# Kernel tuning notes

Measured on AMD Instinct MI355X. Metric: run time of the kernel, lower is better.

## Reference

```python
import jax, jax.numpy as jnp
import numpy as np

B, S, E, H = 2, 1024, 1024, 16
Dh = E // H


def setup_inputs() -> dict:
    key = jax.random.key(0)
    ks = jax.random.split(key, 32)
    sc = 1.0 / np.sqrt(E)  # xavier-ish scale
    inp = {}
    names_x = ["x_q_a", "x_q_b", "x_kv_a", "x_kv_b"]
    for i, n in enumerate(names_x):
        inp[n] = jax.random.normal(ks[i], (B, S, E), jnp.float32)
    # causal mask, broadcastable to (B, H, S, S); masked where == 0
    inp["mask"] = jnp.tril(jnp.ones((S, S), jnp.int32))[None, None, :, :]
    inp["layer_theta"] = jnp.float32(0.3)
    inp["thetas_head"] = 0.1 * jax.random.normal(ks[4], (H,), jnp.float32)
    i = 5
    for p in ["q", "k", "v", "o"]:
        inp[p + "_wa"] = sc * jax.random.normal(ks[i], (E, E), jnp.float32); i += 1
        inp[p + "_wb"] = sc * jax.random.normal(ks[i], (E, E), jnp.float32); i += 1
        inp[p + "_ba"] = jnp.zeros((E,), jnp.float32)
        inp[p + "_bb"] = jnp.zeros((E,), jnp.float32)
    return inp


def _qc_dense(xa, xb, wa, wb, ba, bb, j2):
    # F.linear: x @ W.T + b ; j2 is a scalar so (Wb*j2) factors out
    out_a = xa @ wa.T + ba + (xb @ wb.T) * j2
    out_b = xa @ wb.T + bb + xb @ wa.T
    return out_a, out_b


def _shape(x):
    # (B,S,E) -> (B,H,S,Dh)
    return x.reshape(B, S, H, Dh).transpose(0, 2, 1, 3)


def _unshape(x):
    return x.transpose(0, 2, 1, 3).reshape(B, S, E)


def _rope(x):
    # standard rotate-half RoPE on last dim, positions over axis -2
    inv_freq = 1.0 / (10000.0 ** (jnp.arange(0, Dh, 2, dtype=jnp.float32) / Dh))
    ang = jnp.arange(S, dtype=jnp.float32)[:, None] * inv_freq[None, :]  # (S, Dh/2)
    cos = jnp.concatenate([jnp.cos(ang), jnp.cos(ang)], axis=-1)  # (S, Dh)
    sin = jnp.concatenate([jnp.sin(ang), jnp.sin(ang)], axis=-1)
    x1, x2 = x[..., : Dh // 2], x[..., Dh // 2:]
    rot = jnp.concatenate([-x2, x1], axis=-1)
    return x * cos + rot * sin


def reference(x_q_a, x_q_b, x_kv_a, x_kv_b, mask, layer_theta, thetas_head,
              q_wa, q_wb, q_ba, q_bb, k_wa, k_wb, k_ba, k_bb,
              v_wa, v_wb, v_ba, v_bb, o_wa, o_wb, o_ba, o_bb):
    j2 = jnp.sin(2.0 * layer_theta) - 1.0
    qa, qb = _qc_dense(x_q_a, x_q_b, q_wa, q_wb, q_ba, q_bb, j2)
    ka, kb = _qc_dense(x_kv_a, x_kv_b, k_wa, k_wb, k_ba, k_bb, j2)
    va, vb = _qc_dense(x_kv_a, x_kv_b, v_wa, v_wb, v_ba, v_bb, j2)
    qa, qb = _rope(_shape(qa)), _rope(_shape(qb))
    ka, kb = _rope(_shape(ka)), _rope(_shape(kb))
    va, vb = _shape(va), _shape(vb)
    j2h = (jnp.sin(2.0 * thetas_head) - 1.0).reshape(1, H, 1, 1)
    # dual QC score matrices (B,H,S,S)
    s_a = jnp.einsum("bhqd,bhkd->bhqk", qa, ka) + jnp.einsum("bhqd,bhkd->bhqk", qb, kb) * j2h
    s_b = jnp.einsum("bhqd,bhkd->bhqk", qa, kb) + jnp.einsum("bhqd,bhkd->bhqk", qb, ka)
    mag = jnp.sqrt(s_a * s_a + s_b * s_b + 1e-8) / np.sqrt(Dh)
    mag = jnp.where(mask == 0, -1e9, mag)
    attn = jax.nn.softmax(mag, axis=-1)
    out_a = _unshape(jnp.einsum("bhqk,bhkd->bhqd", attn, va))
    out_b = _unshape(jnp.einsum("bhqk,bhkd->bhqd", attn, vb))
    return _qc_dense(out_a, out_b, o_wa, o_wb, o_ba, o_bb, j2)
```

## Files before the change

kernel.cpp:

```cpp
#include <hip/hip_runtime.h>
#include <math.h>
#include <stdint.h>

#define BATCH 2
#define SEQ   1024
#define EMB   1024
#define NH    16
#define DH    64
#define BSE   (BATCH*SEQ*EMB)
#define MROWS (BATCH*SEQ)

typedef unsigned short u16;
typedef __attribute__((ext_vector_type(8))) short short8;
typedef __attribute__((ext_vector_type(4))) float f32x4;

__device__ __forceinline__ float bf2f(u16 u) {
    return __uint_as_float(((unsigned int)u) << 16);
}
__device__ __forceinline__ u16 f2bf(float f) {
    unsigned int x = __float_as_uint(f);
    x += 0x7FFFu + ((x >> 16) & 1u);
    return (u16)(x >> 16);
}

__device__ __forceinline__ void async_copy16(const void* g, void* l) {
    __builtin_amdgcn_global_load_lds(
        (const __attribute__((address_space(1))) unsigned int*)g,
        (__attribute__((address_space(3))) unsigned int*)l,
        16, 0, 0);
}

struct PackArgs {
    const float* src[20];
    u16*         dst[20];
    int          scaled[20];
};

__global__ __launch_bounds__(256) void pack_kernel(PackArgs pa, const float* __restrict__ theta)
{
    const int e = blockIdx.y;
    const size_t i = ((size_t)blockIdx.x * 256 + threadIdx.x) * 4;
    float sc = 1.0f;
    if (pa.scaled[e]) sc = sinf(2.0f * theta[0]) - 1.0f;
    float4 v = *(const float4*)(pa.src[e] + i);
    ushort4 o;
    o.x = f2bf(v.x * sc); o.y = f2bf(v.y * sc);
    o.z = f2bf(v.z * sc); o.w = f2bf(v.w * sc);
    *(ushort4*)(pa.dst[e] + i) = o;
}

struct GemmArgs {
    const u16*   A1s[8];
    const u16*   A2s[8];
    const u16*   Blo[8];
    const u16*   Bhi[8];
    const float* bias[8];
    void*        dst[8];
    int          mode[8];
};

template<int SPLITK>
__global__ __launch_bounds__(256) void mfma_gemm(GemmArgs ga)
{
    __shared__ u16 sA[128][32];
    __shared__ u16 sB[128][32];

    const int t    = threadIdx.x;
    const int lane = t & 63;
    const int w    = t >> 6;
    const int wx   = w & 1;
    const int wy   = w >> 1;
    const int n0   = blockIdx.y * 128;
    const int m0   = blockIdx.x * 128;
    const int ko   = (SPLITK == 2) ? blockIdx.z : 0;
    const int seg  = n0 >> 10;
    const int nloc = n0 & 1023;

    const int srow = t >> 2;
    const int sb   = (t & 3) * 16;

    f32x4 acc[4][4] = {};

    const char* A1 = (const char*)ga.A1s[seg];
    const char* A2 = (const char*)ga.A2s[seg];
    const char* Bl = (const char*)ga.Blo[seg];
    const char* Bh = (const char*)ga.Bhi[seg];
    if (SPLITK == 2 && ko) { A1 = A2; Bl = Bh; }

    const int frow = lane & 15;
    const int quad = lane >> 4;

    const int NKT = (SPLITK == 2) ? 32 : 64;
    for (int kt = 0; kt < NKT; ++kt) {
        const char* As = (SPLITK == 1 && (kt & 32)) ? A2 : A1;
        const char* Bs = (SPLITK == 1 && (kt & 32)) ? Bh : Bl;
        const size_t kbyte = (size_t)(kt & 31) * 64;

        __syncthreads();
        #pragma unroll
        for (int r = 0; r < 2; ++r) {
            const int row = r*64 + srow;
            const int ldsoff = (r*64 + w*16) * 64;
            async_copy16(As + (size_t)(m0 + row)*2048 + kbyte + sb,
                         (char*)&sA[0][0] + ldsoff);
            async_copy16(Bs + (size_t)(nloc + row)*2048 + kbyte + sb,
                         (char*)&sB[0][0] + ldsoff);
        }
        __syncthreads();

        short8 af[4], bfr[4];
        #pragma unroll
        for (int i = 0; i < 4; ++i)
            af[i] = *(const short8*)&sA[wy*64 + i*16 + frow][quad*8];
        #pragma unroll
        for (int j = 0; j < 4; ++j)
            bfr[j] = *(const short8*)&sB[wx*64 + j*16 + frow][quad*8];

        #pragma unroll
        for (int i = 0; i < 4; ++i)
            #pragma unroll
            for (int j = 0; j < 4; ++j)
                acc[i][j] = __builtin_amdgcn_mfma_f32_16x16x32_bf16(
                                af[i], bfr[j], acc[i][j], 0, 0, 0);
    }

    const float* bias = ga.bias[seg];
    const int mode = ga.mode[seg];

    #pragma unroll
    for (int j = 0; j < 4; ++j) {
        const int c = nloc + wx*64 + j*16 + frow;
        const float bv = (SPLITK == 2 && ko) ? 0.0f : bias[c];
        #pragma unroll
        for (int i = 0; i < 4; ++i) {
            #pragma unroll
            for (int reg = 0; reg < 4; ++reg) {
                const int m = m0 + wy*64 + i*16 + quad*4 + reg;
                const float val = acc[i][j][reg] + bv;
                if (mode == 1) {
                    if (SPLITK == 2)
                        atomicAdd((float*)ga.dst[seg] + (size_t)m*1024 + c, val);
                    else
                        ((float*)ga.dst[seg])[(size_t)m*1024 + c] = val;
                } else if (mode == 2) {
                    ((u16*)ga.dst[seg])[((size_t)(m >> 10) << 20) + (size_t)c*1024 + (m & 1023)] = f2bf(val);
                } else {
                    ((u16*)ga.dst[seg])[(size_t)m*1024 + c] = f2bf(val);
                }
            }
        }
    }
}

__global__ __launch_bounds__(256) void rope_kernel(
    u16* qa, u16* qb, u16* ka, u16* kb)
{
    u16* p;
    switch (blockIdx.y) {
        case 0:  p = qa; break;
        case 1:  p = qb; break;
        case 2:  p = ka; break;
        default: p = kb; break;
    }
    const int i   = blockIdx.x * 256 + threadIdx.x;
    const int d   = i & 31;
    const int hh  = (i >> 5) & (NH - 1);
    const int row = i >> 9;
    const int s   = row & (SEQ - 1);
    const size_t base = (size_t)row * EMB + hh * DH;

    float x1 = bf2f(p[base + d]);
    float x2 = bf2f(p[base + d + 32]);
    const float invf_rev = expf(-(float)d * 0.28782313662425576f) * 0.15915494309189535f;
    float rev = (float)s * invf_rev;
    rev -= floorf(rev);
    const float sn = __builtin_amdgcn_sinf(rev);
    const float cs = __builtin_amdgcn_cosf(rev);
    p[base + d]      = f2bf(x1 * cs - x2 * sn);
    p[base + d + 32] = f2bf(x2 * cs + x1 * sn);
}

__global__ __launch_bounds__(256) void attn_mfma(
    const u16* __restrict__ qa, const u16* __restrict__ qb,
    const u16* __restrict__ ka, const u16* __restrict__ kb,
    const u16* __restrict__ vat, const u16* __restrict__ vbt,
    const float* __restrict__ thetas,
    u16* __restrict__ oa, u16* __restrict__ ob)
{
    __shared__ u16 sKa[64][64];
    __shared__ u16 sKb[64][64];
    __shared__ u16 sVa[64][64];
    __shared__ u16 sVb[64][64];
    __shared__ u16 sP[4][16][72];

    const int t    = threadIdx.x;
    const int lane = t & 63;
    const int w    = t >> 6;
    const int L15  = lane & 15;
    const int quad = lane >> 4;

    const int bid  = blockIdx.x;
    const int aa   = (bid >> 5) & 7;
    const int qt   = (bid >> 8) ? aa : (15 - aa);
    const int bh   = bid & 31;
    const int h    = bh & 15;
    const int b    = bh >> 4;

    const float j2h = sinf(2.0f * thetas[h]) - 1.0f;

    const int   qrow  = qt*64 + w*16 + L15;
    const size_t qbase = (size_t)(b*SEQ + qrow) * EMB + h*DH;
    short8 fqa[2], fqb[2], fjqb[2];
    fqa[0] = *(const short8*)(qa + qbase + quad*8);
    fqa[1] = *(const short8*)(qa + qbase + 32 + quad*8);
    fqb[0] = *(const short8*)(qb + qbase + quad*8);
    fqb[1] = *(const short8*)(qb + qbase + 32 + quad*8);
    #pragma unroll
    for (int s2 = 0; s2 < 2; ++s2) {
        short8 src = fqb[s2], dst;
        #pragma unroll
        for (int j = 0; j < 8; ++j)
            dst[j] = (short)f2bf(bf2f((u16)src[j]) * j2h);
        fjqb[s2] = dst;
    }

    f32x4 acc_a[4] = {};
    f32x4 acc_b[4] = {};
    float l_lane[4] = {0.f, 0.f, 0.f, 0.f};

    const int subrow = lane >> 3;
    const int g      = (lane & 7) ^ subrow;
    const int swz    = L15 & 7;

    for (int kt = 0; kt <= qt; ++kt) {
        __syncthreads();
        #pragma unroll
        for (int i = 0; i < 2; ++i) {
            const int row = w*16 + i*8 + subrow;
            const int ldsoff = (w*16 + i*8) * 128;
            const size_t ktok = (size_t)(b*SEQ + kt*64 + row);
            async_copy16((const char*)ka + ktok*2048 + h*128 + g*16,
                         (char*)&sKa[0][0] + ldsoff);
            async_copy16((const char*)kb + ktok*2048 + h*128 + g*16,
                         (char*)&sKb[0][0] + ldsoff);
            const size_t vrow = (size_t)b*1048576 + (size_t)(h*64 + row)*1024 + kt*64;
            async_copy16((const char*)vat + vrow*2 + g*16,
                         (char*)&sVa[0][0] + ldsoff);
            async_copy16((const char*)vbt + vrow*2 + g*16,
                         (char*)&sVb[0][0] + ldsoff);
        }
        __syncthreads();

        f32x4 sa[4] = {}, sb[4] = {};
        #pragma unroll
        for (int n = 0; n < 4; ++n) {
            const u16* rKa = &sKa[n*16 + L15][0];
            const u16* rKb = &sKb[n*16 + L15][0];
            short8 ka0 = *(const short8*)(rKa + (( quad      ^ swz) << 3));
            short8 ka1 = *(const short8*)(rKa + (((4 + quad) ^ swz) << 3));
            short8 kb0 = *(const short8*)(rKb + (( quad      ^ swz) << 3));
            short8 kb1 = *(const short8*)(rKb + (((4 + quad) ^ swz) << 3));
            sa[n] = __builtin_amdgcn_mfma_f32_16x16x32_bf16(fqa[0],  ka0, sa[n], 0, 0, 0);
            sa[n] = __builtin_amdgcn_mfma_f32_16x16x32_bf16(fqa[1],  ka1, sa[n], 0, 0, 0);
            sa[n] = __builtin_amdgcn_mfma_f32_16x16x32_bf16(fjqb[0], kb0, sa[n], 0, 0, 0);
            sa[n] = __builtin_amdgcn_mfma_f32_16x16x32_bf16(fjqb[1], kb1, sa[n], 0, 0, 0);
            sb[n] = __builtin_amdgcn_mfma_f32_16x16x32_bf16(fqa[0],  kb0, sb[n], 0, 0, 0);
            sb[n] = __builtin_amdgcn_mfma_f32_16x16x32_bf16(fqa[1],  kb1, sb[n], 0, 0, 0);
            sb[n] = __builtin_amdgcn_mfma_f32_16x16x32_bf16(fqb[0],  ka0, sb[n], 0, 0, 0);
            sb[n] = __builtin_amdgcn_mfma_f32_16x16x32_bf16(fqb[1],  ka1, sb[n], 0, 0, 0);
        }

        float p[4][4];
        if (kt == qt) {
            #pragma unroll
            for (int n = 0; n < 4; ++n)
                #pragma unroll
                for (int r = 0; r < 4; ++r) {
                    const float A = sa[n][r], B = sb[n][r];
                    const float mag = __builtin_amdgcn_sqrtf(A*A + B*B + 1e-8f) * 0.125f;
                    const bool masked = (n*16 + L15) > (w*16 + quad*4 + r);
                    p[n][r] = masked ? 0.0f
                                     : __builtin_amdgcn_exp2f(mag * 1.44269504f);
                }
        } else {
            #pragma unroll
            for (int n = 0; n < 4; ++n)
                #pragma unroll
                for (int r = 0; r < 4; ++r) {
                    const float A = sa[n][r], B = sb[n][r];
                    const float mag = __builtin_amdgcn_sqrtf(A*A + B*B + 1e-8f) * 0.125f;
                    p[n][r] = __builtin_amdgcn_exp2f(mag * 1.44269504f);
                }
        }
        #pragma unroll
        for (int r = 0; r < 4; ++r)
            l_lane[r] += (p[0][r] + p[1][r]) + (p[2][r] + p[3][r]);

        #pragma unroll
        for (int n = 0; n < 4; ++n)
            #pragma unroll
            for (int r = 0; r < 4; ++r)
                sP[w][quad*4 + r][n*16 + L15] = f2bf(p[n][r]);

        short8 pf0 = *(const short8*)&sP[w][L15][quad*8];
        short8 pf1 = *(const short8*)&sP[w][L15][32 + quad*8];

        #pragma unroll
        for (int n = 0; n < 4; ++n) {
            const u16* rVa = &sVa[n*16 + L15][0];
            const u16* rVb = &sVb[n*16 + L15][0];
            short8 va0 = *(const short8*)(rVa + (( quad      ^ swz) << 3));
            short8 va1 = *(const short8*)(rVa + (((4 + quad) ^ swz) << 3));
            short8 vb0 = *(const short8*)(rVb + (( quad      ^ swz) << 3));
            short8 vb1 = *(const short8*)(rVb + (((4 + quad) ^ swz) << 3));
            acc_a[n] = __builtin_amdgcn_mfma_f32_16x16x32_bf16(pf0, va0, acc_a[n], 0, 0, 0);
            acc_a[n] = __builtin_amdgcn_mfma_f32_16x16x32_bf16(pf1, va1, acc_a[n], 0, 0, 0);
            acc_b[n] = __builtin_amdgcn_mfma_f32_16x16x32_bf16(pf0, vb0, acc_b[n], 0, 0, 0);
            acc_b[n] = __builtin_amdgcn_mfma_f32_16x16x32_bf16(pf1, vb1, acc_b[n], 0, 0, 0);
        }
    }

    float inv[4];
    #pragma unroll
    for (int r = 0; r < 4; ++r) {
        float l = l_lane[r];
        #pragma unroll
        for (int off = 8; off >= 1; off >>= 1)
            l += __shfl_xor(l, off, 64);
        inv[r] = 1.0f / l;
    }

    #pragma unroll
    for (int reg = 0; reg < 4; ++reg) {
        const size_t tok = (size_t)(b*SEQ + qt*64 + w*16 + quad*4 + reg);
        #pragma unroll
        for (int n = 0; n < 4; ++n) {
            const size_t idx = tok*EMB + h*DH + n*16 + L15;
            oa[idx] = f2bf(acc_a[n][reg] * inv[reg]);
            ob[idx] = f2bf(acc_b[n][reg] * inv[reg]);
        }
    }
}

extern "C" void kernel_launch(void* const* d_in, const int* in_sizes, int n_in,
                              void* d_out, int out_size, void* d_ws, size_t ws_size,
                              hipStream_t stream)
{
    const float* x_q_a  = (const float*)d_in[0];
    const float* x_q_b  = (const float*)d_in[1];
    const float* x_kv_a = (const float*)d_in[2];
    const float* x_kv_b = (const float*)d_in[3];
    const float* theta    = (const float*)d_in[5];
    const float* thetas_h = (const float*)d_in[6];
    const float* q_wa = (const float*)d_in[7];
    const float* q_wb = (const float*)d_in[8];
    const float* q_ba = (const float*)d_in[9];
    const float* q_bb = (const float*)d_in[10];
    const float* k_wa = (const float*)d_in[11];
    const float* k_wb = (const float*)d_in[12];
    const float* k_ba = (const float*)d_in[13];
    const float* k_bb = (const float*)d_in[14];
    const float* v_wa = (const float*)d_in[15];
    const float* v_wb = (const float*)d_in[16];
    const float* v_ba = (const float*)d_in[17];
    const float* v_bb = (const float*)d_in[18];
    const float* o_wa = (const float*)d_in[19];
    const float* o_wb = (const float*)d_in[20];
    const float* o_ba = (const float*)d_in[21];
    const float* o_bb = (const float*)d_in[22];

    u16* W = (u16*)d_ws;
    const size_t XN = (size_t)BSE;
    const size_t WN = (size_t)EMB*EMB;
    u16* xq_a16  = W;
    u16* xq_b16  = W + XN;
    u16* xkv_a16 = W + 2*XN;
    u16* xkv_b16 = W + 3*XN;
    u16* wbase   = W + 4*XN;
    u16* q_wa16  = wbase;
    u16* q_wb16  = wbase + WN;
    u16* k_wa16  = wbase + 2*WN;
    u16* k_wb16  = wbase + 3*WN;
    u16* v_wa16  = wbase + 4*WN;
    u16* v_wb16  = wbase + 5*WN;
    u16* o_wa16  = wbase + 6*WN;
    u16* o_wb16  = wbase + 7*WN;
    u16* q_wbs16 = wbase + 8*WN;
    u16* k_wbs16 = wbase + 9*WN;
    u16* v_wbs16 = wbase + 10*WN;
    u16* o_wbs16 = wbase + 11*WN;
    u16* qkv     = wbase + 12*WN;
    u16* qa16 = qkv;
    u16* qb16 = qkv + XN;
    u16* ka16 = qkv + 2*XN;
    u16* kb16 = qkv + 3*XN;
    u16* vat16 = qkv + 4*XN;
    u16* vbt16 = qkv + 5*XN;
    u16* ao16 = xq_a16;
    u16* bo16 = xq_b16;

    float* out_a = (float*)d_out;
    float* out_b = out_a + (size_t)BSE;

    PackArgs pa;
    int si = 0;
    auto add = [&](const float* s, u16* d, int scaled, int chunks) {
        for (int c = 0; c < chunks; ++c) {
            pa.src[si] = s + (size_t)c * WN;
            pa.dst[si] = d + (size_t)c * WN;
            pa.scaled[si] = scaled;
            ++si;
        }
    };
    add(x_q_a,  xq_a16,  0, 2);
    add(x_q_b,  xq_b16,  0, 2);
    add(x_kv_a, xkv_a16, 0, 2);
    add(x_kv_b, xkv_b16, 0, 2);
    add(q_wa, q_wa16, 0, 1);  add(q_wb, q_wb16, 0, 1);
    add(k_wa, k_wa16, 0, 1);  add(k_wb, k_wb16, 0, 1);
    add(v_wa, v_wa16, 0, 1);  add(v_wb, v_wb16, 0, 1);
    add(o_wa, o_wa16, 0, 1);  add(o_wb, o_wb16, 0, 1);
    add(q_wb, q_wbs16, 1, 1); add(k_wb, k_wbs16, 1, 1);
    add(v_wb, v_wbs16, 1, 1); add(o_wb, o_wbs16, 1, 1);
    pack_kernel<<<dim3(WN/1024, 20), 256, 0, stream>>>(pa, theta);

    hipMemsetAsync(d_out, 0, (size_t)out_size * sizeof(float), stream);

    GemmArgs g12;
    const u16* a1s[6] = { xq_a16, xq_a16, xkv_a16, xkv_a16, xkv_a16, xkv_a16 };
    const u16* a2s[6] = { xq_b16, xq_b16, xkv_b16, xkv_b16, xkv_b16, xkv_b16 };
    const u16* blo[6] = { q_wa16, q_wb16, k_wa16, k_wb16, v_wa16, v_wb16 };
    const u16* bhi[6] = { q_wbs16, q_wa16, k_wbs16, k_wa16, v_wbs16, v_wa16 };
    const float* bia[6] = { q_ba, q_bb, k_ba, k_bb, v_ba, v_bb };
    void* dsts[6] = { qa16, qb16, ka16, kb16, vat16, vbt16 };
    const int modes[6] = { 0, 0, 0, 0, 2, 2 };
    for (int s = 0; s < 6; ++s) {
        g12.A1s[s] = a1s[s]; g12.A2s[s] = a2s[s];
        g12.Blo[s] = blo[s]; g12.Bhi[s] = bhi[s];
        g12.bias[s] = bia[s]; g12.dst[s] = dsts[s]; g12.mode[s] = modes[s];
    }
    for (int s = 6; s < 8; ++s) {
        g12.A1s[s] = a1s[0]; g12.A2s[s] = a2s[0];
        g12.Blo[s] = blo[0]; g12.Bhi[s] = bhi[0];
        g12.bias[s] = bia[0]; g12.dst[s] = dsts[0]; g12.mode[s] = 0;
    }
    mfma_gemm<1><<<dim3(MROWS/128, 48), 256, 0, stream>>>(g12);

    rope_kernel<<<dim3((BATCH*SEQ*NH*32)/256, 4), 256, 0, stream>>>(qa16, qb16, ka16, kb16);

    attn_mfma<<<BATCH*NH*(SEQ/64), 256, 0, stream>>>(qa16, qb16, ka16, kb16,
                                                     vat16, vbt16, thetas_h, ao16, bo16);

    GemmArgs g3;
    for (int s = 0; s < 8; ++s) {
        g3.A1s[s] = ao16; g3.A2s[s] = bo16;
        g3.Blo[s] = o_wa16; g3.Bhi[s] = o_wbs16;
        g3.bias[s] = o_ba; g3.dst[s] = out_a; g3.mode[s] = 1;
    }
    g3.Blo[1] = o_wb16; g3.Bhi[1] = o_wa16; g3.bias[1] = o_bb; g3.dst[1] = out_b;
    mfma_gemm<2><<<dim3(MROWS/128, 16, 2), 256, 0, stream>>>(g3);
}
```

Measured before the change: 314.7 us.

## Replace QKV projection GEMM with 256x256-tile 8-wave pipelined MFMA kernel

Adds a new QKV projection GEMM that uses 256x256 output tiles and 512 threads. It double-buffers K-slices in swizzled LDS, loaded with async global-to-LDS copies, and staged in quarter-steps separated by vmcnt waits and barriers. Blocks are mapped XCD-aware, so each XCD handles a contiguous group of N tiles, and MFMA bursts get raised priority. The goal is more data reuse per tile and better overlap of loads with MFMA than the old 128-row tile kernel. The trade-off is higher LDS and register use, and only 192 blocks for the whole projection.

```diff
diff --git a/kernel.cpp b/kernel.cpp
--- a/kernel.cpp
+++ b/kernel.cpp
@@ -29,6 +29,11 @@
         (__attribute__((address_space(3))) unsigned int*)l,
         16, 0, 0);
 }
+
+#define VMCNT(N)  asm volatile("s_waitcnt vmcnt(" #N ")" ::: "memory")
+#define BARRIER_SYNC() do { asm volatile("" ::: "memory"); \
+                            __builtin_amdgcn_s_barrier();  \
+                            asm volatile("" ::: "memory"); } while (0)
 
 struct PackArgs {
     const float* src[20];
@@ -47,6 +52,207 @@
     o.x = f2bf(v.x * sc); o.y = f2bf(v.y * sc);
     o.z = f2bf(v.z * sc); o.w = f2bf(v.w * sc);
     *(ushort4*)(pa.dst[e] + i) = o;
+}
+
+struct Gemm8Args {
+    const u16*   A1s[6];
+    const u16*   A2s[6];
+    const u16*   Blo[6];
+    const u16*   Bhi[6];
+    const float* bias[6];
+    void*        dst[6];
+    int          mode[6];
+};
+
+__global__ __launch_bounds__(512, 2) void mfma_gemm8(Gemm8Args ga)
+{
+    __shared__ u16 lds[2][2][256][64];
+
+    const int t    = threadIdx.x;
+    const int lane = t & 63;
+    const int w    = t >> 6;
+    const int wm   = w >> 2;
+    const int wn   = w & 3;
+    const int L15  = lane & 15;
+    const int quad = lane >> 4;
+    const int rswz = L15 & 7;
+
+    const int bid = blockIdx.x;
+    const int xcd = bid & 7;
+    const int idx = bid >> 3;
+    const int nt  = xcd * 3 + (idx >> 3);
+    const int mt  = idx & 7;
+    const int m0   = mt * 256;
+    const int seg  = nt >> 2;
+    const int nloc = (nt & 3) * 256;
+
+    const char* A1 = (const char*)ga.A1s[seg];
+    const char* A2 = (const char*)ga.A2s[seg];
+    const char* Bl = (const char*)ga.Blo[seg];
+    const char* Bh = (const char*)ga.Bhi[seg];
+
+    const int   srow8 = t >> 3;
+    const int   g16   = (((t & 7) ^ (srow8 & 7)) << 4);
+    const char* A1t = A1 + (size_t)(m0   + srow8) * 2048 + g16;
+    const char* A2t = A2 + (size_t)(m0   + srow8) * 2048 + g16;
+    const char* Blt = Bl + (size_t)(nloc + srow8) * 2048 + g16;
+    const char* Bht = Bh + (size_t)(nloc + srow8) * 2048 + g16;
+    char* ldsW = (char*)&lds[0][0][0][0] + w * 1024;
+
+    auto stage_half = [&](int buf, int mat, const char* srcT, size_t kcol, int r0) {
+        #pragma unroll
+        for (int c = 0; c < 2; ++c)
+            async_copy16(srcT + (size_t)(r0 + c*64) * 2048 + kcol,
+                         ldsW + buf*65536 + mat*32768 + (r0 + c*64)*128);
+    };
+
+    auto ldA = [&](const u16* Abw, int mq, int m, int ks) -> short8 {
+        return *(const short8*)(Abw + (mq*128 + m*16)*64 + (((ks*4 + quad) ^ rswz) << 3));
+    };
+    auto ldB = [&](const u16* Bbw, int nq, int n, int ks) -> short8 {
+        return *(const short8*)(Bbw + (nq*128 + n*16)*64 + (((ks*4 + quad) ^ rswz) << 3));
+    };
+
+    f32x4 acc00[4][2] = {};
+    f32x4 acc01[4][2] = {};
+    f32x4 acc11[4][2] = {};
+    f32x4 acc10[4][2] = {};
+    short8 fa[4][2];
+    short8 fb0[2][2];
+    short8 fb1[2][2];
+
+    auto mfma4x2 = [&](f32x4 (&accq)[4][2], short8 (&a)[4][2], short8 (&b)[2][2]) {
+        __builtin_amdgcn_s_setprio(1);
+        #pragma unroll
+        for (int m = 0; m < 4; ++m)
+            #pragma unroll
+            for (int n = 0; n < 2; ++n) {
+                accq[m][n] = __builtin_amdgcn_mfma_f32_16x16x32_bf16(a[m][0], b[n][0], accq[m][n], 0, 0, 0);
+                accq[m][n] = __builtin_amdgcn_mfma_f32_16x16x32_bf16(a[m][1], b[n][1], accq[m][n], 0, 0, 0);
+            }
+        __builtin_amdgcn_s_setprio(0);
+    };
+
+    stage_half(0, 0, A1t, 0, 0);
+    stage_half(0, 1, Blt, 0, 0);
+    stage_half(0, 1, Blt, 0, 128);
+    stage_half(0, 0, A1t, 0, 128);
+
+    for (int kt = 0; kt < 31; ++kt) {
+        const int cur = kt & 1, nxt = cur ^ 1;
+        const bool hi = ((kt + 1) & 16) != 0;
+        const char* At = hi ? A2t : A1t;
+        const char* Bt = hi ? Bht : Blt;
+        const size_t kc = (size_t)((kt + 1) & 15) * 128;
+        const u16* Abw = &lds[cur][0][wm*64 + L15][0];
+        const u16* Bbw = &lds[cur][1][wn*32 + L15][0];
+
+        stage_half(nxt, 0, At, kc, 0);
+        VMCNT(6);
+        BARRIER_SYNC();
+        #pragma unroll
+        for (int m = 0; m < 4; ++m)
+            #pragma unroll
+            for (int ks = 0; ks < 2; ++ks)
+                fa[m][ks] = ldA(Abw, 0, m, ks);
+        #pragma unroll
+        for (int n = 0; n < 2; ++n)
+            #pragma unroll
+            for (int ks = 0; ks < 2; ++ks)
+                fb0[n][ks] = ldB(Bbw, 0, n, ks);
+        mfma4x2(acc00, fa, fb0);
+
+        stage_half(nxt, 1, Bt, kc, 0);
+        VMCNT(6);
+        BARRIER_SYNC();
+        #pragma unroll
+        for (int n = 0; n < 2; ++n)
+            #pragma unroll
+            for (int ks = 0; ks < 2; ++ks)
+                fb1[n][ks] = ldB(Bbw, 1, n, ks);
+        mfma4x2(acc01, fa, fb1);
+
+        stage_half(nxt, 1, Bt, kc, 128);
+        VMCNT(6);
+        BARRIER_SYNC();
+        #pragma unroll
+        for (int m = 0; m < 4; ++m)
+            #pragma unroll
+            for (int ks = 0; ks < 2; ++ks)
+                fa[m][ks] = ldA(Abw, 1, m, ks);
+        mfma4x2(acc11, fa, fb1);
+
+        stage_half(nxt, 0, At, kc, 128);
+        mfma4x2(acc10, fa, fb0);
+    }
+
+    {
+        const u16* Abw = &lds[1][0][wm*64 + L15][0];
+        const u16* Bbw = &lds[1][1][wn*32 + L15][0];
+
+        VMCNT(4);
+        BARRIER_SYNC();
+        #pragma unroll
+        for (int m = 0; m < 4; ++m)
+            #pragma unroll
+            for (int ks = 0; ks < 2; ++ks)
+                fa[m][ks] = ldA(Abw, 0, m, ks);
+        #pragma unroll
+        for (int n = 0; n < 2; ++n)
+            #pragma unroll
+            for (int ks = 0; ks < 2; ++ks)
+                fb0[n][ks] = ldB(Bbw, 0, n, ks);
+        mfma4x2(acc00, fa, fb0);
+
+        VMCNT(2);
+        BARRIER_SYNC();
+        #pragma unroll
+        for (int n = 0; n < 2; ++n)
+            #pragma unroll
+            for (int ks = 0; ks < 2; ++ks)
+                fb1[n][ks] = ldB(Bbw, 1, n, ks);
+        mfma4x2(acc01, fa, fb1);
+
+        VMCNT(0);
+        BARRIER_SYNC();
+        #pragma unroll
+        for (int m = 0; m < 4; ++m)
+            #pragma unroll
+            for (int ks = 0; ks < 2; ++ks)
+                fa[m][ks] = ldA(Abw, 1, m, ks);
+        mfma4x2(acc11, fa, fb1);
+
+        mfma4x2(acc10, fa, fb0);
+    }
+
+    const float* bias = ga.bias[seg];
+    const int mode = ga.mode[seg];
+    u16* dst = (u16*)ga.dst[seg];
+
+    auto store_quad = [&](f32x4 (&accq)[4][2], int mq, int nq) {
+        #pragma unroll
+        for (int n = 0; n < 2; ++n) {
+            const int c = nloc + nq*128 + wn*32 + n*16 + L15;
+            const float bv = bias[c];
+            #pragma unroll
+            for (int m = 0; m < 4; ++m) {
+                #pragma unroll
+                for (int reg = 0; reg < 4; ++reg) {
+                    const int row = m0 + mq*128 + wm*64 + m*16 + quad*4 + reg;
+                    const float val = accq[m][n][reg] + bv;
+                    if (mode == 2) {
+                        dst[((size_t)(row >> 10) << 20) + (size_t)c*1024 + (row & 1023)] = f2bf(val);
+                    } else {
+                        dst[(size_t)row*1024 + c] = f2bf(val);
+                    }
+                }
+            }
+        }
+    };
+    store_quad(acc00, 0, 0);
+    store_quad(acc01, 0, 1);
+    store_quad(acc11, 1, 1);
+    store_quad(acc10, 1, 0);
 }
 
 struct GemmArgs {
@@ -426,25 +632,22 @@
 
     hipMemsetAsync(d_out, 0, (size_t)out_size * sizeof(float), stream);
 
-    GemmArgs g12;
-    const u16* a1s[6] = { xq_a16, xq_a16, xkv_a16, xkv_a16, xkv_a16, xkv_a16 };
-    const u16* a2s[6] = { xq_b16, xq_b16, xkv_b16, xkv_b16, xkv_b16, xkv_b16 };
-    const u16* blo[6] = { q_wa16, q_wb16, k_wa16, k_wb16, v_wa16, v_wb16 };
-    const u16* bhi[6] = { q_wbs16, q_wa16, k_wbs16, k_wa16, v_wbs16, v_wa16 };
-    const float* bia[6] = { q_ba, q_bb, k_ba, k_bb, v_ba, v_bb };
-    void* dsts[6] = { qa16, qb16, ka16, kb16, vat16, vbt16 };
-    const int modes[6] = { 0, 0, 0, 0, 2, 2 };
-    for (int s = 0; s < 6; ++s) {
-        g12.A1s[s] = a1s[s]; g12.A2s[s] = a2s[s];
-        g12.Blo[s] = blo[s]; g12.Bhi[s] = bhi[s];
-        g12.bias[s] = bia[s]; g12.dst[s] = dsts[s]; g12.mode[s] = modes[s];
-    }
-    for (int s = 6; s < 8; ++s) {
-        g12.A1s[s] = a1s[0]; g12.A2s[s] = a2s[0];
-        g12.Blo[s] = blo[0]; g12.Bhi[s] = bhi[0];
-        g12.bias[s] = bia[0]; g12.dst[s] = dsts[0]; g12.mode[s] = 0;
-    }
-    mfma_gemm<1><<<dim3(MROWS/128, 48), 256, 0, stream>>>(g12);
+    Gemm8Args g8;
+    {
+        const u16* a1s[6] = { xq_a16, xq_a16, xkv_a16, xkv_a16, xkv_a16, xkv_a16 };
+        const u16* a2s[6] = { xq_b16, xq_b16, xkv_b16, xkv_b16, xkv_b16, xkv_b16 };
+        const u16* blo[6] = { q_wa16, q_wb16, k_wa16, k_wb16, v_wa16, v_wb16 };
+        const u16* bhi[6] = { q_wbs16, q_wa16, k_wbs16, k_wa16, v_wbs16, v_wa16 };
+        const float* bia[6] = { q_ba, q_bb, k_ba, k_bb, v_ba, v_bb };
+        void* dsts[6] = { qa16, qb16, ka16, kb16, vat16, vbt16 };
+        const int modes[6] = { 0, 0, 0, 0, 2, 2 };
+        for (int s = 0; s < 6; ++s) {
+            g8.A1s[s] = a1s[s]; g8.A2s[s] = a2s[s];
+            g8.Blo[s] = blo[s]; g8.Bhi[s] = bhi[s];
+            g8.bias[s] = bia[s]; g8.dst[s] = dsts[s]; g8.mode[s] = modes[s];
+        }
+    }
+    mfma_gemm8<<<dim3(192), 512, 0, stream>>>(g8);
 
     rope_kernel<<<dim3((BATCH*SEQ*NH*32)/256, 4), 256, 0, stream>>>(qa16, qb16, ka16, kb16);
 
```

New measurement: 313.5 us. About the same (-0.4%).

## Fuse RoPE into QKV GEMM epilogue and fold output zeroing into pack kernel

Applied to the files above, without the earlier changes.

Applies the rotate-half RoPE directly in the projection GEMM epilogue for the Q and K outputs, using each wave's 64-column tile so that the paired columns d and d+32 sit in the same thread's accumulators. This drops the separate rope kernel and its bf16 read-modify-write pass over four activation tensors. Zeroing of the split-K atomic output buffer moves from hipMemsetAsync into extra blocks of the pack kernel, removing one launch. The epilogue now does more transcendental work per element, and its correctness depends on the wave tile lining up with head boundaries.

```diff
diff --git a/kernel.cpp b/kernel.cpp
--- a/kernel.cpp
+++ b/kernel.cpp
@@ -31,17 +31,23 @@
 }
 
 struct PackArgs {
-    const float* src[20];
-    u16*         dst[20];
-    int          scaled[20];
+    const float* src[24];
+    u16*         dst[24];
+    int          scaled[24];
 };
 
 __global__ __launch_bounds__(256) void pack_kernel(PackArgs pa, const float* __restrict__ theta)
 {
     const int e = blockIdx.y;
     const size_t i = ((size_t)blockIdx.x * 256 + threadIdx.x) * 4;
+    const int sc_mode = pa.scaled[e];
+    if (sc_mode == 2) {
+        float4 z = {0.f, 0.f, 0.f, 0.f};
+        *(float4*)((float*)pa.dst[e] + i) = z;
+        return;
+    }
     float sc = 1.0f;
-    if (pa.scaled[e]) sc = sinf(2.0f * theta[0]) - 1.0f;
+    if (sc_mode == 1) sc = sinf(2.0f * theta[0]) - 1.0f;
     float4 v = *(const float4*)(pa.src[e] + i);
     ushort4 o;
     o.x = f2bf(v.x * sc); o.y = f2bf(v.y * sc);
@@ -126,6 +132,36 @@
 
     const float* bias = ga.bias[seg];
     const int mode = ga.mode[seg];
+
+    if (mode == 3) {
+        u16* dst = (u16*)ga.dst[seg];
+        #pragma unroll
+        for (int j = 0; j < 2; ++j) {
+            const int c1 = nloc + wx*64 + j*16 + frow;
+            const int c2 = c1 + 32;
+            const float bv1 = bias[c1];
+            const float bv2 = bias[c2];
+            const int d = j*16 + frow;
+            const float invf_rev = expf(-(float)d * 0.28782313662425576f) * 0.15915494309189535f;
+            #pragma unroll
+            for (int i = 0; i < 4; ++i) {
+                #pragma unroll
+                for (int reg = 0; reg < 4; ++reg) {
+                    const int m = m0 + wy*64 + i*16 + quad*4 + reg;
+                    const int s = m & (SEQ - 1);
+                    float rev = (float)s * invf_rev;
+                    rev -= floorf(rev);
+                    const float sn = __builtin_amdgcn_sinf(rev);
+                    const float cs = __builtin_amdgcn_cosf(rev);
+                    const float x1 = acc[i][j][reg]   + bv1;
+                    const float x2 = acc[i][j+2][reg] + bv2;
+                    dst[(size_t)m*1024 + c1] = f2bf(x1*cs - x2*sn);
+                    dst[(size_t)m*1024 + c2] = f2bf(x2*cs + x1*sn);
+                }
+            }
+        }
+        return;
+    }
 
     #pragma unroll
     for (int j = 0; j < 4; ++j) {
@@ -150,34 +186,6 @@
             }
         }
     }
-}
-
-__global__ __launch_bounds__(256) void rope_kernel(
-    u16* qa, u16* qb, u16* ka, u16* kb)
-{
-    u16* p;
-    switch (blockIdx.y) {
-        case 0:  p = qa; break;
-        case 1:  p = qb; break;
-        case 2:  p = ka; break;
-        default: p = kb; break;
-    }
-    const int i   = blockIdx.x * 256 + threadIdx.x;
-    const int d   = i & 31;
-    const int hh  = (i >> 5) & (NH - 1);
-    const int row = i >> 9;
-    const int s   = row & (SEQ - 1);
-    const size_t base = (size_t)row * EMB + hh * DH;
-
-    float x1 = bf2f(p[base + d]);
-    float x2 = bf2f(p[base + d + 32]);
-    const float invf_rev = expf(-(float)d * 0.28782313662425576f) * 0.15915494309189535f;
-    float rev = (float)s * invf_rev;
-    rev -= floorf(rev);
-    const float sn = __builtin_amdgcn_sinf(rev);
-    const float cs = __builtin_amdgcn_cosf(rev);
-    p[base + d]      = f2bf(x1 * cs - x2 * sn);
-    p[base + d + 32] = f2bf(x2 * cs + x1 * sn);
 }
 
 __global__ __launch_bounds__(256) void attn_mfma(
@@ -406,8 +414,8 @@
     int si = 0;
     auto add = [&](const float* s, u16* d, int scaled, int chunks) {
         for (int c = 0; c < chunks; ++c) {
-            pa.src[si] = s + (size_t)c * WN;
-            pa.dst[si] = d + (size_t)c * WN;
+            pa.src[si] = s ? (s + (size_t)c * WN) : nullptr;
+            pa.dst[si] = d + (size_t)c * WN * (scaled == 2 ? 2 : 1);
             pa.scaled[si] = scaled;
             ++si;
         }
@@ -422,9 +430,8 @@
     add(o_wa, o_wa16, 0, 1);  add(o_wb, o_wb16, 0, 1);
     add(q_wb, q_wbs16, 1, 1); add(k_wb, k_wbs16, 1, 1);
     add(v_wb, v_wbs16, 1, 1); add(o_wb, o_wbs16, 1, 1);
-    pack_kernel<<<dim3(WN/1024, 20), 256, 0, stream>>>(pa, theta);
-
-    hipMemsetAsync(d_out, 0, (size_t)out_size * sizeof(float), stream);
+    add(nullptr, (u16*)d_out, 2, 4);
+    pack_kernel<<<dim3(WN/1024, 24), 256, 0, stream>>>(pa, theta);
 
     GemmArgs g12;
     const u16* a1s[6] = { xq_a16, xq_a16, xkv_a16, xkv_a16, xkv_a16, xkv_a16 };
@@ -433,7 +440,7 @@
     const u16* bhi[6] = { q_wbs16, q_wa16, k_wbs16, k_wa16, v_wbs16, v_wa16 };
     const float* bia[6] = { q_ba, q_bb, k_ba, k_bb, v_ba, v_bb };
     void* dsts[6] = { qa16, qb16, ka16, kb16, vat16, vbt16 };
-    const int modes[6] = { 0, 0, 0, 0, 2, 2 };
+    const int modes[6] = { 3, 3, 3, 3, 2, 2 };
     for (int s = 0; s < 6; ++s) {
         g12.A1s[s] = a1s[s]; g12.A2s[s] = a2s[s];
         g12.Blo[s] = blo[s]; g12.Bhi[s] = bhi[s];
@@ -445,8 +452,6 @@
         g12.bias[s] = bia[0]; g12.dst[s] = dsts[0]; g12.mode[s] = 0;
     }
     mfma_gemm<1><<<dim3(MROWS/128, 48), 256, 0, stream>>>(g12);
-
-    rope_kernel<<<dim3((BATCH*SEQ*NH*32)/256, 4), 256, 0, stream>>>(qa16, qb16, ka16, kb16);
 
     attn_mfma<<<BATCH*NH*(SEQ/64), 256, 0, stream>>>(qa16, qb16, ka16, kb16,
                                                      vat16, vbt16, thetas_h, ao16, bo16);
```

Measured after the change: 327.0 us. +3.9%, slower.
